# Kernel optimization log

Hardware: AMD Instinct MI355X
Metric: run time of the kernel (lower is better)

The kernel has to match this reference:

```python
import jax, jax.numpy as jnp
import numpy as np

# Dimensions: batch B, seq S, in_features I, num_stripes N, stripe_size Q
B, S, I, N, Q = 2, 512, 4096, 32, 128
OUT = N * Q  # out_features == out_slice (divides evenly)


def setup_inputs() -> dict:
    key = jax.random.key(0)
    k0, k1, k2, k3 = jax.random.split(key, 4)
    x = jax.random.normal(k0, (B, S, I), jnp.float32)
    # kernel scaled like fan_in variance-scaling init
    W_kernel = jax.random.normal(k1, (I, OUT), jnp.float32) / np.float32(np.sqrt(I))
    # positive thresholds in [0,1): with |x| half-normal this gives partial stripe occupancy
    thresholds = jax.random.uniform(k2, (I, N), jnp.float32)
    mu = jnp.zeros((I,), jnp.float32)  # dist_tracker.adj_med_computed buffer
    out_mu = jax.random.normal(k3, (OUT,), jnp.float32) * 0.05  # out_mu_computed buffer
    where = jnp.ones((B, S), bool)
    return {"x": x, "W_kernel": W_kernel, "thresholds": thresholds,
            "mu": mu, "out_mu": out_mu, "where": where}


def reference(x, W_kernel, thresholds, mu, out_mu, where):
    # Eval-mode CWICDense forward (train_mode=False, the module default).
    x_off = x - mu                                   # [B,S,I]
    gate = jnp.abs(x_off)[..., None]                 # [B,S,I,1]
    # soft_jump eval: occupance = (gate >= threshold); z = x_off * occupance
    z = jnp.where(gate >= thresholds, x_off[..., None], jnp.zeros((), x.dtype))  # [B,S,I,N]
    Wr = W_kernel.reshape(I, N, Q)                   # stripe-partitioned kernel
    y = jnp.einsum('bsin,inq->bsnq', z, Wr)          # conditional stripe matmul
    y = y.reshape(B, S, OUT) + out_mu                # add precomputed W(mu) offset
    return y[..., :OUT]                              # out_slice == OUT (no-op slice)
```

## Files before the change

kernel.cpp:

```cpp
#include <hip/hip_runtime.h>
#include <hip/hip_bf16.h>
#include <stdint.h>

#define R_TOTAL 1024
#define I_DIM   4096
#define OUT_DIM 4096
#define N_STR   32
#define Q_DIM   128

typedef __attribute__((ext_vector_type(8))) __bf16 bf16x8;
typedef __attribute__((ext_vector_type(4))) float  f32x4;

__device__ __forceinline__ ushort f2bf(float f) {
    uint32_t u = __float_as_uint(f);
    uint32_t r = (u + 0x7fffu + ((u >> 16) & 1u)) >> 16;
    return (ushort)r;
}

__device__ __forceinline__ float bf2f(ushort u) {
    return __uint_as_float((uint32_t)u << 16);
}

__device__ __forceinline__ uint32_t bexp(uint32_t b, int w) {
    return ((b >> (2 * w)) & 1u) * 0xFFFFu | ((b >> (2 * w + 1)) & 1u) * 0xFFFF0000u;
}

__device__ __forceinline__ void async16(void* lds, const void* g) {
    __builtin_amdgcn_global_load_lds(
        (const __attribute__((address_space(1))) unsigned int*)g,
        (__attribute__((address_space(3))) unsigned int*)lds, 16, 0, 0);
}


__device__ __forceinline__ void transpose_w_block(const float* __restrict__ W,
                                                  ushort* __restrict__ WT,
                                                  int c0, int i0, int t,
                                                  float (*tile)[65]) {
    {
        int dc4 = (t & 15) * 4;
        int di  = t >> 4;
        #pragma unroll
        for (int p = 0; p < 4; ++p) {
            int ii = di + p * 16;
            float4 v = *(const float4*)(W + (size_t)(i0 + ii) * OUT_DIM + c0 + dc4);
            tile[ii][dc4 + 0] = v.x; tile[ii][dc4 + 1] = v.y;
            tile[ii][dc4 + 2] = v.z; tile[ii][dc4 + 3] = v.w;
        }
    }
    __syncthreads();
    {
        int iq = (t & 15) * 4;
        int dc = t >> 4;
        #pragma unroll
        for (int p = 0; p < 4; ++p) {
            int cc = dc + p * 16;
            ushort4 o;
            o.x = f2bf(tile[iq + 0][cc]);
            o.y = f2bf(tile[iq + 1][cc]);
            o.z = f2bf(tile[iq + 2][cc]);
            o.w = f2bf(tile[iq + 3][cc]);
            *(ushort4*)(WT + (size_t)(c0 + cc) * I_DIM + i0 + iq) = o;
        }
    }
}

__device__ __forceinline__ void prep_block4(const float* __restrict__ x,
                                            const float* __restrict__ mu,
                                            const float* __restrict__ th,
                                            ushort* __restrict__ XB,
                                            unsigned long long* __restrict__ MB64,
                                            int rb, int ib, int tid,
                                            char* smem) {
    ushort* sXB = (ushort*)smem;
    unsigned long long* sMB = (unsigned long long*)(smem + 4096);
    int i = ib * 256 + tid;
    int lane = tid & 63;
    int wave = tid >> 6;

    float4 tq[8];
    #pragma unroll
    for (int q = 0; q < 8; ++q)
        tq[q] = *(const float4*)(th + (size_t)i * N_STR + q * 4);

    float muv = mu[i];
    float ax[8];
    #pragma unroll
    for (int rr = 0; rr < 8; ++rr) {
        float xo = x[(size_t)(rb * 8 + rr) * I_DIM + i] - muv;
        sXB[rr * 256 + tid] = f2bf(xo);
        ax[rr] = fabsf(xo);
    }

    #pragma unroll
    for (int n = 0; n < N_STR; ++n) {
        float4 v = tq[n >> 2];
        float tn = (n & 3) == 0 ? v.x : (n & 3) == 1 ? v.y : (n & 3) == 2 ? v.z : v.w;
        unsigned long long bal[8];
        #pragma unroll
        for (int rr = 0; rr < 8; ++rr)
            bal[rr] = __ballot(ax[rr] >= tn);
        if (lane == 0) {
            #pragma unroll
            for (int rr = 0; rr < 8; ++rr)
                sMB[(n * 4 + wave) * 8 + rr] = bal[rr];
        }
    }
    __syncthreads();

    {
        int row = tid >> 5, seg = tid & 31;
        uint4 v = *(const uint4*)&sXB[row * 256 + seg * 8];
        *(uint4*)(XB + (size_t)(rb * 8 + row) * I_DIM + ib * 256 + seg * 8) = v;
    }
    {
        int n = tid >> 3, rr = tid & 7;
        unsigned long long v0 = sMB[(n * 4 + 0) * 8 + rr];
        unsigned long long v1 = sMB[(n * 4 + 1) * 8 + rr];
        unsigned long long v2 = sMB[(n * 4 + 2) * 8 + rr];
        unsigned long long v3 = sMB[(n * 4 + 3) * 8 + rr];
        unsigned long long* dst = MB64 + ((size_t)n * R_TOTAL + rb * 8 + rr) * 64 + ib * 4;
        dst[0] = v0; dst[1] = v1; dst[2] = v2; dst[3] = v3;
    }
}

__global__ __launch_bounds__(256) void k_prep6(const float* __restrict__ W,
                                               ushort* __restrict__ WT,
                                               const float* __restrict__ x,
                                               const float* __restrict__ mu,
                                               const float* __restrict__ th,
                                               ushort* __restrict__ XB,
                                               unsigned long long* __restrict__ MB64) {
    __shared__ __align__(16) float smem[64 * 65];
    int b = blockIdx.x;
    int t = threadIdx.x;
    int g = b / 3;
    int r = b - g * 3;
    if (r == 2) {
        prep_block4(x, mu, th, XB, MB64, g >> 4, g & 15, t, (char*)smem);
    } else {
        int tb = g * 2 + r;
        transpose_w_block(W, WT, (tb & 63) * 64, (tb >> 6) * 64, t,
                          (float (*)[65])smem);
    }
}


__global__ __launch_bounds__(256, 3) void k_main9(const ushort* __restrict__ XB,
                                                  const ushort* __restrict__ WT,
                                                  const uint8_t* __restrict__ MB,
                                                  ushort* __restrict__ PB0,
                                                  ushort* __restrict__ PB1,
                                                  ushort* __restrict__ PB2) {
    __shared__ ushort sA[128 * 64];
    __shared__ ushort sB[2][128 * 64];

    int bid  = blockIdx.x;
    int xcd  = bid & 7;
    int slot = bid >> 3;
    int n    = xcd * 4 + (slot & 3);
    int rt   = (slot >> 2) & 7;
    int kq   = slot >> 5;
    int r0   = rt * 128;
    int k0   = (kq == 0) ? 0 : (kq == 1) ? 1408 : 2752;
    int NT   = (kq == 0) ? 22 : 21;
    int cbase = n * Q_DIM;
    ushort* P = (kq == 0) ? PB0 : (kq == 1) ? PB1 : PB2;

    int tid  = threadIdx.x;
    int lane = tid & 63;
    int wave = tid >> 6;
    int wr   = wave >> 1;
    int wc   = wave & 1;
    int lrow = lane & 15;
    int lgrp = lane >> 4;

    const ushort*  pXA[4];
    const uint8_t* pMA[4];
    int awz[4];
    {
        int ar = tid >> 3;
        int ak = (tid & 7) * 8;
        #pragma unroll
        for (int p = 0; p < 4; ++p) {
            int row = p * 32 + ar;
            pXA[p] = XB + (size_t)(r0 + row) * I_DIM + k0 + ak;
            pMA[p] = MB + ((size_t)n * R_TOTAL + r0 + row) * 512 + (k0 >> 3) + (tid & 7);
            awz[p] = row * 128 + ((ak * 2) ^ ((row & 7) << 4));
        }
    }

    const char* pBq[4];
    int ldsBo[4];
    #pragma unroll
    for (int q = 0; q < 4; ++q) {
        int chunk = wave * 4 + q;
        int col = chunk * 8 + (lane >> 3);
        pBq[q] = (const char*)WT + (size_t)(cbase + col) * (I_DIM * 2)
               + (size_t)k0 * 2 + (((lane & 7) ^ (lane >> 3)) << 4);
        ldsBo[q] = chunk * 1024;
    }

    f32x4 acc[4][4];
    #pragma unroll
    for (int m2 = 0; m2 < 4; ++m2)
        #pragma unroll
        for (int nn = 0; nn < 4; ++nn)
            acc[m2][nn] = (f32x4){0.f, 0.f, 0.f, 0.f};

    uint4 va[4]; uint32_t mk[4];

    #pragma unroll
    for (int p = 0; p < 4; ++p) { va[p] = *(const uint4*)pXA[p]; mk[p] = *pMA[p]; }
    #pragma unroll
    for (int q = 0; q < 4; ++q) async16((char*)sB[0] + ldsBo[q], pBq[q]);
    #pragma unroll
    for (int p = 0; p < 4; ++p) {
        uint4 z;
        z.x = va[p].x & bexp(mk[p], 0); z.y = va[p].y & bexp(mk[p], 1);
        z.z = va[p].z & bexp(mk[p], 2); z.w = va[p].w & bexp(mk[p], 3);
        *(uint4*)((char*)sA + awz[p]) = z;
    }
    #pragma unroll
    for (int p = 0; p < 4; ++p) { va[p] = *(const uint4*)(pXA[p] + 64); mk[p] = *(pMA[p] + 8); }
    __syncthreads();

    for (int t = 0; t < NT; ++t) {
        if (t + 1 < NT) {
            #pragma unroll
            for (int q = 0; q < 4; ++q)
                async16((char*)sB[(t + 1) & 1] + ldsBo[q],
                        pBq[q] + (size_t)(t + 1) * 128);
        }
        const char* sAc = (const char*)sA;
        const char* sBc = (const char*)sB[t & 1];
        __builtin_amdgcn_s_setprio(1);
        #pragma unroll
        for (int ks = 0; ks < 2; ++ks) {
            int kb = ks * 64 + (lgrp << 4);
            bf16x8 af[4], bfr[4];
            #pragma unroll
            for (int m2 = 0; m2 < 4; ++m2) {
                int row = wr * 64 + m2 * 16 + lrow;
                af[m2] = *(const bf16x8*)(sAc + row * 128 + (kb ^ ((row & 7) << 4)));
            }
            #pragma unroll
            for (int nn = 0; nn < 4; ++nn) {
                int col = wc * 64 + nn * 16 + lrow;
                bfr[nn] = *(const bf16x8*)(sBc + col * 128 + (kb ^ ((col & 7) << 4)));
            }
            #pragma unroll
            for (int m2 = 0; m2 < 4; ++m2)
                #pragma unroll
                for (int nn = 0; nn < 4; ++nn)
                    acc[m2][nn] = __builtin_amdgcn_mfma_f32_16x16x32_bf16(af[m2], bfr[nn], acc[m2][nn], 0, 0, 0);
        }
        __builtin_amdgcn_s_setprio(0);
        __syncthreads();
        if (t + 1 < NT) {
            #pragma unroll
            for (int p = 0; p < 4; ++p) {
                uint4 z;
                z.x = va[p].x & bexp(mk[p], 0); z.y = va[p].y & bexp(mk[p], 1);
                z.z = va[p].z & bexp(mk[p], 2); z.w = va[p].w & bexp(mk[p], 3);
                *(uint4*)((char*)sA + awz[p]) = z;
            }
            if (t + 2 < NT) {
                #pragma unroll
                for (int p = 0; p < 4; ++p) {
                    va[p] = *(const uint4*)(pXA[p] + (size_t)(t + 2) * 64);
                    mk[p] = *(pMA[p] + (size_t)(t + 2) * 8);
                }
            }
        }
        __syncthreads();
    }

    #pragma unroll
    for (int nn = 0; nn < 4; ++nn) {
        int col = cbase + wc * 64 + nn * 16 + lrow;
        #pragma unroll
        for (int m2 = 0; m2 < 4; ++m2) {
            int rbase = r0 + wr * 64 + m2 * 16 + lgrp * 4;
            #pragma unroll
            for (int j = 0; j < 4; ++j)
                P[(size_t)(rbase + j) * OUT_DIM + col] = f2bf(acc[m2][nn][j]);
        }
    }
}

__global__ __launch_bounds__(256) void k_reduce3b(float* __restrict__ out,
                                                  const ushort* __restrict__ PB0,
                                                  const ushort* __restrict__ PB1,
                                                  const ushort* __restrict__ PB2,
                                                  const float* __restrict__ out_mu) {
    int idx = blockIdx.x * 256 + threadIdx.x;
    uint4 a = *(const uint4*)(PB0 + (size_t)idx * 8);
    uint4 b = *(const uint4*)(PB1 + (size_t)idx * 8);
    uint4 c = *(const uint4*)(PB2 + (size_t)idx * 8);
    const float* om = out_mu + (idx & 511) * 8;
    float4 m0 = *(const float4*)om;
    float4 m1 = *(const float4*)(om + 4);
    float4 o0, o1;
    o0.x = bf2f((ushort)(a.x & 0xFFFF)) + bf2f((ushort)(b.x & 0xFFFF)) + bf2f((ushort)(c.x & 0xFFFF)) + m0.x;
    o0.y = bf2f((ushort)(a.x >> 16))    + bf2f((ushort)(b.x >> 16))    + bf2f((ushort)(c.x >> 16))    + m0.y;
    o0.z = bf2f((ushort)(a.y & 0xFFFF)) + bf2f((ushort)(b.y & 0xFFFF)) + bf2f((ushort)(c.y & 0xFFFF)) + m0.z;
    o0.w = bf2f((ushort)(a.y >> 16))    + bf2f((ushort)(b.y >> 16))    + bf2f((ushort)(c.y >> 16))    + m0.w;
    o1.x = bf2f((ushort)(a.z & 0xFFFF)) + bf2f((ushort)(b.z & 0xFFFF)) + bf2f((ushort)(c.z & 0xFFFF)) + m1.x;
    o1.y = bf2f((ushort)(a.z >> 16))    + bf2f((ushort)(b.z >> 16))    + bf2f((ushort)(c.z >> 16))    + m1.y;
    o1.z = bf2f((ushort)(a.w & 0xFFFF)) + bf2f((ushort)(b.w & 0xFFFF)) + bf2f((ushort)(c.w & 0xFFFF)) + m1.z;
    o1.w = bf2f((ushort)(a.w >> 16))    + bf2f((ushort)(b.w >> 16))    + bf2f((ushort)(c.w >> 16))    + m1.w;
    float* dst = out + (size_t)idx * 8;
    *(float4*)dst = o0;
    *(float4*)(dst + 4) = o1;
}

__global__ __launch_bounds__(256) void k_naive(const float* __restrict__ x,
                                               const float* __restrict__ W,
                                               const float* __restrict__ th,
                                               const float* __restrict__ mu,
                                               const float* __restrict__ out_mu,
                                               float* __restrict__ out) {
    int idx = blockIdx.x * 256 + threadIdx.x;
    int r = idx >> 12;
    int c = idx & 4095;
    int n = c >> 7;
    float s = 0.f;
    for (int i = 0; i < I_DIM; ++i) {
        float xo = x[(size_t)r * I_DIM + i] - mu[i];
        if (fabsf(xo) >= th[i * N_STR + n])
            s += xo * W[(size_t)i * OUT_DIM + c];
    }
    out[idx] = s + out_mu[c];
}

extern "C" void kernel_launch(void* const* d_in, const int* in_sizes, int n_in,
                              void* d_out, int out_size, void* d_ws, size_t ws_size,
                              hipStream_t stream) {
    const float* x      = (const float*)d_in[0];
    const float* W      = (const float*)d_in[1];
    const float* th     = (const float*)d_in[2];
    const float* mu     = (const float*)d_in[3];
    const float* out_mu = (const float*)d_in[4];
    float* out = (float*)d_out;

    const size_t wT_b = (size_t)OUT_DIM * I_DIM * sizeof(ushort);
    const size_t xb_b = (size_t)R_TOTAL * I_DIM * sizeof(ushort);
    const size_t mb_b = (size_t)N_STR * R_TOTAL * 512;
    const size_t pb_b = (size_t)R_TOTAL * OUT_DIM * sizeof(ushort);

    ushort*  WT  = (ushort*)d_ws;
    ushort*  XBp = (ushort*)((char*)d_ws + wT_b);
    uint8_t* MBp = (uint8_t*)((char*)d_ws + wT_b + xb_b);
    ushort*  PB0 = (ushort*)((char*)d_ws + wT_b + xb_b + mb_b);
    ushort*  PB1 = (ushort*)((char*)d_ws + wT_b + xb_b + mb_b + pb_b);
    ushort*  PB2 = (ushort*)((char*)d_ws + wT_b + xb_b + mb_b + 2 * pb_b);

    if (ws_size >= wT_b + xb_b + mb_b + 3 * pb_b) {
        k_prep6<<<6144, 256, 0, stream>>>(W, WT, x, mu, th, XBp,
                                          (unsigned long long*)MBp);
        k_main9<<<768, 256, 0, stream>>>(XBp, WT, MBp, PB0, PB1, PB2);
        k_reduce3b<<<(R_TOTAL * OUT_DIM / 8) / 256, 256, 0, stream>>>(out, PB0, PB1, PB2, out_mu);
    } else {
        k_naive<<<(R_TOTAL * OUT_DIM) / 256, 256, 0, stream>>>(x, W, th, mu, out_mu, out);
    }
}
```

Measured before the change: 102.3 us.

## Fuse gating into main GEMM, replacing precomputed bf16 x and bitmask with transposed thresholds

The prep kernel no longer converts x to bf16 or builds per-stripe ballot bitmasks. It now transposes W and the thresholds (to [N, I]), and the main kernel reads fp32 x, mu and thresholds directly, applying the gate and packing to bf16 in registers with v_cvt_pk_bf16_f32. This removes a prep pass and the mask and bf16-x workspace traffic. The cost is that each main block loads fp32 x, twice the bytes of the bf16 copy, and redoes the subtract/compare/convert work across the 32 stripes and 3 K-split passes.

```diff
diff --git a/kernel.cpp b/kernel.cpp
--- a/kernel.cpp
+++ b/kernel.cpp
@@ -21,8 +21,15 @@
     return __uint_as_float((uint32_t)u << 16);
 }
 
-__device__ __forceinline__ uint32_t bexp(uint32_t b, int w) {
-    return ((b >> (2 * w)) & 1u) * 0xFFFFu | ((b >> (2 * w + 1)) & 1u) * 0xFFFF0000u;
+__device__ __forceinline__ uint32_t gate_pk(float x0, float x1,
+                                            float m0, float m1,
+                                            float t0, float t1) {
+    float a = x0 - m0, b = x1 - m1;
+    float ga = (fabsf(a) >= t0) ? a : 0.f;
+    float gb = (fabsf(b) >= t1) ? b : 0.f;
+    uint32_t r;
+    asm("v_cvt_pk_bf16_f32 %0, %1, %2" : "=v"(r) : "v"(ga), "v"(gb));
+    return r;
 }
 
 __device__ __forceinline__ void async16(void* lds, const void* g) {
@@ -64,93 +71,57 @@
     }
 }
 
-__device__ __forceinline__ void prep_block4(const float* __restrict__ x,
-                                            const float* __restrict__ mu,
-                                            const float* __restrict__ th,
-                                            ushort* __restrict__ XB,
-                                            unsigned long long* __restrict__ MB64,
-                                            int rb, int ib, int tid,
-                                            char* smem) {
-    ushort* sXB = (ushort*)smem;
-    unsigned long long* sMB = (unsigned long long*)(smem + 4096);
-    int i = ib * 256 + tid;
-    int lane = tid & 63;
-    int wave = tid >> 6;
-
-    float4 tq[8];
-    #pragma unroll
-    for (int q = 0; q < 8; ++q)
-        tq[q] = *(const float4*)(th + (size_t)i * N_STR + q * 4);
-
-    float muv = mu[i];
-    float ax[8];
-    #pragma unroll
-    for (int rr = 0; rr < 8; ++rr) {
-        float xo = x[(size_t)(rb * 8 + rr) * I_DIM + i] - muv;
-        sXB[rr * 256 + tid] = f2bf(xo);
-        ax[rr] = fabsf(xo);
-    }
-
-    #pragma unroll
-    for (int n = 0; n < N_STR; ++n) {
-        float4 v = tq[n >> 2];
-        float tn = (n & 3) == 0 ? v.x : (n & 3) == 1 ? v.y : (n & 3) == 2 ? v.z : v.w;
-        unsigned long long bal[8];
-        #pragma unroll
-        for (int rr = 0; rr < 8; ++rr)
-            bal[rr] = __ballot(ax[rr] >= tn);
-        if (lane == 0) {
-            #pragma unroll
-            for (int rr = 0; rr < 8; ++rr)
-                sMB[(n * 4 + wave) * 8 + rr] = bal[rr];
-        }
+__device__ __forceinline__ void transpose_th_block(const float* __restrict__ th,
+                                                   float* __restrict__ thT,
+                                                   int i0, int t, float* tile) {
+    {
+        int ri = t >> 2;
+        int nc = (t & 3) * 8;
+        float4 v0 = *(const float4*)(th + (size_t)(i0 + ri) * N_STR + nc);
+        float4 v1 = *(const float4*)(th + (size_t)(i0 + ri) * N_STR + nc + 4);
+        tile[ri * 33 + nc + 0] = v0.x; tile[ri * 33 + nc + 1] = v0.y;
+        tile[ri * 33 + nc + 2] = v0.z; tile[ri * 33 + nc + 3] = v0.w;
+        tile[ri * 33 + nc + 4] = v1.x; tile[ri * 33 + nc + 5] = v1.y;
+        tile[ri * 33 + nc + 6] = v1.z; tile[ri * 33 + nc + 7] = v1.w;
     }
     __syncthreads();
-
-    {
-        int row = tid >> 5, seg = tid & 31;
-        uint4 v = *(const uint4*)&sXB[row * 256 + seg * 8];
-        *(uint4*)(XB + (size_t)(rb * 8 + row) * I_DIM + ib * 256 + seg * 8) = v;
-    }
-    {
-        int n = tid >> 3, rr = tid & 7;
-        unsigned long long v0 = sMB[(n * 4 + 0) * 8 + rr];
-        unsigned long long v1 = sMB[(n * 4 + 1) * 8 + rr];
-        unsigned long long v2 = sMB[(n * 4 + 2) * 8 + rr];
-        unsigned long long v3 = sMB[(n * 4 + 3) * 8 + rr];
-        unsigned long long* dst = MB64 + ((size_t)n * R_TOTAL + rb * 8 + rr) * 64 + ib * 4;
-        dst[0] = v0; dst[1] = v1; dst[2] = v2; dst[3] = v3;
-    }
-}
-
-__global__ __launch_bounds__(256) void k_prep6(const float* __restrict__ W,
+    {
+        int n  = t >> 3;
+        int di = (t & 7) * 8;
+        float4 o0, o1;
+        o0.x = tile[(di + 0) * 33 + n]; o0.y = tile[(di + 1) * 33 + n];
+        o0.z = tile[(di + 2) * 33 + n]; o0.w = tile[(di + 3) * 33 + n];
+        o1.x = tile[(di + 4) * 33 + n]; o1.y = tile[(di + 5) * 33 + n];
+        o1.z = tile[(di + 6) * 33 + n]; o1.w = tile[(di + 7) * 33 + n];
+        *(float4*)(thT + (size_t)n * I_DIM + i0 + di) = o0;
+        *(float4*)(thT + (size_t)n * I_DIM + i0 + di + 4) = o1;
+    }
+}
+
+__global__ __launch_bounds__(256) void k_prep7(const float* __restrict__ W,
                                                ushort* __restrict__ WT,
-                                               const float* __restrict__ x,
-                                               const float* __restrict__ mu,
                                                const float* __restrict__ th,
-                                               ushort* __restrict__ XB,
-                                               unsigned long long* __restrict__ MB64) {
+                                               float* __restrict__ thT) {
     __shared__ __align__(16) float smem[64 * 65];
     int b = blockIdx.x;
     int t = threadIdx.x;
-    int g = b / 3;
-    int r = b - g * 3;
-    if (r == 2) {
-        prep_block4(x, mu, th, XB, MB64, g >> 4, g & 15, t, (char*)smem);
+    if (b < 64) {
+        transpose_th_block(th, thT, b * 64, t, smem);
     } else {
-        int tb = g * 2 + r;
+        int tb = b - 64;
         transpose_w_block(W, WT, (tb & 63) * 64, (tb >> 6) * 64, t,
                           (float (*)[65])smem);
     }
 }
 
 
-__global__ __launch_bounds__(256, 3) void k_main9(const ushort* __restrict__ XB,
-                                                  const ushort* __restrict__ WT,
-                                                  const uint8_t* __restrict__ MB,
-                                                  ushort* __restrict__ PB0,
-                                                  ushort* __restrict__ PB1,
-                                                  ushort* __restrict__ PB2) {
+__global__ __launch_bounds__(256, 3) void k_main10(const float* __restrict__ x,
+                                                   const ushort* __restrict__ WT,
+                                                   const float* __restrict__ thT,
+                                                   const float* __restrict__ mu,
+                                                   ushort* __restrict__ PB0,
+                                                   ushort* __restrict__ PB1,
+                                                   ushort* __restrict__ PB2) {
     __shared__ ushort sA[128 * 64];
     __shared__ ushort sB[2][128 * 64];
 
@@ -174,20 +145,20 @@
     int lrow = lane & 15;
     int lgrp = lane >> 4;
 
-    const ushort*  pXA[4];
-    const uint8_t* pMA[4];
+    const float* pX[4];
     int awz[4];
+    const int ak = (tid & 7) * 8;
     {
         int ar = tid >> 3;
-        int ak = (tid & 7) * 8;
         #pragma unroll
         for (int p = 0; p < 4; ++p) {
             int row = p * 32 + ar;
-            pXA[p] = XB + (size_t)(r0 + row) * I_DIM + k0 + ak;
-            pMA[p] = MB + ((size_t)n * R_TOTAL + r0 + row) * 512 + (k0 >> 3) + (tid & 7);
+            pX[p] = x + (size_t)(r0 + row) * I_DIM + k0 + ak;
             awz[p] = row * 128 + ((ak * 2) ^ ((row & 7) << 4));
         }
     }
+    const float* pTH = thT + (size_t)n * I_DIM + k0 + ak;
+    const float* pMU = mu + k0 + ak;
 
     const char* pBq[4];
     int ldsBo[4];
@@ -207,21 +178,33 @@
         for (int nn = 0; nn < 4; ++nn)
             acc[m2][nn] = (f32x4){0.f, 0.f, 0.f, 0.f};
 
-    uint4 va[4]; uint32_t mk[4];
-
-    #pragma unroll
-    for (int p = 0; p < 4; ++p) { va[p] = *(const uint4*)pXA[p]; mk[p] = *pMA[p]; }
+    float4 xa[4][2], thv[2], muv[2];
+
+    #pragma unroll
+    for (int p = 0; p < 4; ++p) {
+        xa[p][0] = *(const float4*)pX[p];
+        xa[p][1] = *((const float4*)pX[p] + 1);
+    }
+    thv[0] = *(const float4*)pTH; thv[1] = *((const float4*)pTH + 1);
+    muv[0] = *(const float4*)pMU; muv[1] = *((const float4*)pMU + 1);
     #pragma unroll
     for (int q = 0; q < 4; ++q) async16((char*)sB[0] + ldsBo[q], pBq[q]);
     #pragma unroll
     for (int p = 0; p < 4; ++p) {
         uint4 z;
-        z.x = va[p].x & bexp(mk[p], 0); z.y = va[p].y & bexp(mk[p], 1);
-        z.z = va[p].z & bexp(mk[p], 2); z.w = va[p].w & bexp(mk[p], 3);
+        z.x = gate_pk(xa[p][0].x, xa[p][0].y, muv[0].x, muv[0].y, thv[0].x, thv[0].y);
+        z.y = gate_pk(xa[p][0].z, xa[p][0].w, muv[0].z, muv[0].w, thv[0].z, thv[0].w);
+        z.z = gate_pk(xa[p][1].x, xa[p][1].y, muv[1].x, muv[1].y, thv[1].x, thv[1].y);
+        z.w = gate_pk(xa[p][1].z, xa[p][1].w, muv[1].z, muv[1].w, thv[1].z, thv[1].w);
         *(uint4*)((char*)sA + awz[p]) = z;
     }
     #pragma unroll
-    for (int p = 0; p < 4; ++p) { va[p] = *(const uint4*)(pXA[p] + 64); mk[p] = *(pMA[p] + 8); }
+    for (int p = 0; p < 4; ++p) {
+        xa[p][0] = *(const float4*)(pX[p] + 64);
+        xa[p][1] = *((const float4*)(pX[p] + 64) + 1);
+    }
+    thv[0] = *(const float4*)(pTH + 64); thv[1] = *((const float4*)(pTH + 64) + 1);
+    muv[0] = *(const float4*)(pMU + 64); muv[1] = *((const float4*)(pMU + 64) + 1);
     __syncthreads();
 
     for (int t = 0; t < NT; ++t) {
@@ -260,16 +243,23 @@
             #pragma unroll
             for (int p = 0; p < 4; ++p) {
                 uint4 z;
-                z.x = va[p].x & bexp(mk[p], 0); z.y = va[p].y & bexp(mk[p], 1);
-                z.z = va[p].z & bexp(mk[p], 2); z.w = va[p].w & bexp(mk[p], 3);
+                z.x = gate_pk(xa[p][0].x, xa[p][0].y, muv[0].x, muv[0].y, thv[0].x, thv[0].y);
+                z.y = gate_pk(xa[p][0].z, xa[p][0].w, muv[0].z, muv[0].w, thv[0].z, thv[0].w);
+                z.z = gate_pk(xa[p][1].x, xa[p][1].y, muv[1].x, muv[1].y, thv[1].x, thv[1].y);
+                z.w = gate_pk(xa[p][1].z, xa[p][1].w, muv[1].z, muv[1].w, thv[1].z, thv[1].w);
                 *(uint4*)((char*)sA + awz[p]) = z;
             }
             if (t + 2 < NT) {
+                int off = (t + 2) * 64;
                 #pragma unroll
                 for (int p = 0; p < 4; ++p) {
-                    va[p] = *(const uint4*)(pXA[p] + (size_t)(t + 2) * 64);
-                    mk[p] = *(pMA[p] + (size_t)(t + 2) * 8);
+                    xa[p][0] = *(const float4*)(pX[p] + off);
+                    xa[p][1] = *((const float4*)(pX[p] + off) + 1);
                 }
+                thv[0] = *(const float4*)(pTH + off);
+                thv[1] = *((const float4*)(pTH + off) + 1);
+                muv[0] = *(const float4*)(pMU + off);
+                muv[1] = *((const float4*)(pMU + off) + 1);
             }
         }
         __syncthreads();
@@ -343,22 +333,19 @@
     const float* out_mu = (const float*)d_in[4];
     float* out = (float*)d_out;
 
-    const size_t wT_b = (size_t)OUT_DIM * I_DIM * sizeof(ushort);
-    const size_t xb_b = (size_t)R_TOTAL * I_DIM * sizeof(ushort);
-    const size_t mb_b = (size_t)N_STR * R_TOTAL * 512;
-    const size_t pb_b = (size_t)R_TOTAL * OUT_DIM * sizeof(ushort);
-
-    ushort*  WT  = (ushort*)d_ws;
-    ushort*  XBp = (ushort*)((char*)d_ws + wT_b);
-    uint8_t* MBp = (uint8_t*)((char*)d_ws + wT_b + xb_b);
-    ushort*  PB0 = (ushort*)((char*)d_ws + wT_b + xb_b + mb_b);
-    ushort*  PB1 = (ushort*)((char*)d_ws + wT_b + xb_b + mb_b + pb_b);
-    ushort*  PB2 = (ushort*)((char*)d_ws + wT_b + xb_b + mb_b + 2 * pb_b);
-
-    if (ws_size >= wT_b + xb_b + mb_b + 3 * pb_b) {
-        k_prep6<<<6144, 256, 0, stream>>>(W, WT, x, mu, th, XBp,
-                                          (unsigned long long*)MBp);
-        k_main9<<<768, 256, 0, stream>>>(XBp, WT, MBp, PB0, PB1, PB2);
+    const size_t wT_b  = (size_t)OUT_DIM * I_DIM * sizeof(ushort);
+    const size_t thT_b = (size_t)N_STR * I_DIM * sizeof(float);
+    const size_t pb_b  = (size_t)R_TOTAL * OUT_DIM * sizeof(ushort);
+
+    ushort* WT  = (ushort*)d_ws;
+    float*  thT = (float*)((char*)d_ws + wT_b);
+    ushort* PB0 = (ushort*)((char*)d_ws + wT_b + thT_b);
+    ushort* PB1 = (ushort*)((char*)d_ws + wT_b + thT_b + pb_b);
+    ushort* PB2 = (ushort*)((char*)d_ws + wT_b + thT_b + 2 * pb_b);
+
+    if (ws_size >= wT_b + thT_b + 3 * pb_b) {
+        k_prep7<<<64 + 4096, 256, 0, stream>>>(W, WT, th, thT);
+        k_main10<<<768, 256, 0, stream>>>(x, WT, thT, mu, PB0, PB1, PB2);
         k_reduce3b<<<(R_TOTAL * OUT_DIM / 8) / 256, 256, 0, stream>>>(out, PB0, PB1, PB2, out_mu);
     } else {
         k_naive<<<(R_TOTAL * OUT_DIM) / 256, 256, 0, stream>>>(x, W, th, mu, out_mu, out);
```

Measured after the change: 87.33 us. -14.6%, faster.
